# Kernel tuning notes

Hardware: AMD Instinct MI355X
Metric: run time of the kernel (lower is better)

## Reference

```python
import jax, jax.numpy as jnp
import numpy as np

B, T, D, H, E, K = 4, 1024, 1024, 16, 8, 2
HS = D // H
DFF = 4 * D
N = B * T
CAP_MAX = N * K // E  # static upper bound on expert capacity (all tokens non-skip)
SKIP_THR = 0.5
LN_EPS = 1e-5


def _ln(x, g, b):
    m = x.mean(-1, keepdims=True)
    v = x.var(-1, keepdims=True)  # biased, matches torch LayerNorm
    return (x - m) * jax.lax.rsqrt(v + LN_EPS) * g + b


def setup_inputs() -> dict:
    key = jax.random.key(0)
    ks = jax.random.split(key, 20)
    s = 0.02
    nrm = lambda k, shp: jax.random.normal(k, shp, dtype=jnp.float32) * s
    return {
        "x": jax.random.normal(ks[0], (B, T, D), dtype=jnp.float32),
        "noise": jax.random.normal(ks[1], (B, T, E), dtype=jnp.float32),
        "ln1_g": jnp.ones((D,), jnp.float32), "ln1_b": jnp.zeros((D,), jnp.float32),
        "wq": nrm(ks[2], (D, D)), "wk": nrm(ks[3], (D, D)), "wv": nrm(ks[4], (D, D)),
        "w_proj": nrm(ks[5], (D, D)), "b_proj": jnp.zeros((D,), jnp.float32),
        "ln2_g": jnp.ones((D,), jnp.float32), "ln2_b": jnp.zeros((D,), jnp.float32),
        "w_router": nrm(ks[6], (D, E)), "b_router": jnp.zeros((E,), jnp.float32),
        "w_noise": nrm(ks[7], (D, E)), "b_noise": jnp.zeros((E,), jnp.float32),
        "w_skip": nrm(ks[8], (D, 1)), "b_skip": jnp.zeros((1,), jnp.float32),
        "ew1": nrm(ks[9], (E, D, DFF)), "eb1": jnp.zeros((E, DFF), jnp.float32),
        "ew2": nrm(ks[10], (E, DFF, D)), "eb2": jnp.zeros((E, D), jnp.float32),
    }


def _block(x, noise, ln1_g, ln1_b, wq, wk, wv, w_proj, b_proj, ln2_g, ln2_b,
           w_router, b_router, w_noise, b_noise, w_skip, b_skip, ew1, eb1, ew2, eb2):
    # ---- multi-head causal self-attention (dropout is identity in eval) ----
    h = _ln(x, ln1_g, ln1_b)
    q = (h @ wq).reshape(B, T, H, HS)
    k = (h @ wk).reshape(B, T, H, HS)
    v = (h @ wv).reshape(B, T, H, HS)
    # NOTE: original scales by C**-0.5 with C = n_embed (not head_size)
    wei = jnp.einsum("bqhd,bkhd->bhqk", q, k) * (D ** -0.5)
    tril = jnp.tril(jnp.ones((T, T), bool))
    wei = jnp.where(tril, wei, -jnp.inf)
    wei = jax.nn.softmax(wei, axis=-1)
    attn = jnp.einsum("bhqk,bkhd->bqhd", wei, v).reshape(B, T, D)
    x1 = x + attn @ w_proj + b_proj

    # ---- cross-layer sparse MoE with skip routing ----
    h2 = _ln(x1, ln2_g, ln2_b)
    logits = h2 @ w_router + b_router                      # [B,T,E]
    noisy = logits + noise * jax.nn.softplus(h2 @ w_noise + b_noise)
    vals, idx = jax.lax.top_k(noisy, K)                    # [B,T,K]
    sparse = jnp.full_like(noisy, -jnp.inf)
    bi = jnp.arange(B)[:, None, None]
    ti = jnp.arange(T)[None, :, None]
    sparse = sparse.at[bi, ti, idx].set(vals)
    gates = jax.nn.softmax(sparse, axis=-1)                # [B,T,E]
    skip = (jax.nn.sigmoid(h2 @ w_skip + b_skip)[..., 0] > SKIP_THR)  # [B,T]

    fx = h2.reshape(N, D)
    fg = gates.reshape(N, E)
    fi = idx.reshape(N, K)
    nsk = ~skip.reshape(N)                                  # non-skip tokens
    n_ns = nsk.sum()
    capacity = (n_ns * K) // E                              # floor(tokens*K/E * 1.0)

    # per-expert dispatch with first-come capacity truncation (flat-token order)
    mask = (fi[None, :, :] == jnp.arange(E)[:, None, None]).any(-1) & nsk[None, :]  # [E,N]
    rank = jnp.cumsum(mask, axis=1) - 1                     # arrival order among non-skip
    within = mask & (rank < capacity)
    slot = jnp.where(within, rank, CAP_MAX)
    buf = jnp.full((E, CAP_MAX + 1), N, dtype=jnp.int32)
    buf = buf.at[jnp.arange(E)[:, None], slot].set(jnp.arange(N, dtype=jnp.int32)[None, :])
    tok = buf[:, :CAP_MAX]                                  # [E,CAP_MAX] token id or N (pad)
    valid = tok < N

    xp = jnp.concatenate([fx, jnp.zeros((1, D), fx.dtype)], axis=0)
    xin = xp[tok]                                           # [E,CAP_MAX,D]
    mid = jax.nn.relu(jnp.einsum("ecd,edf->ecf", xin, ew1) + eb1[:, None, :])
    yout = jnp.einsum("ecf,efd->ecd", mid, ew2) + eb2[:, None, :]
    gp = jnp.concatenate([fg, jnp.zeros((1, E), fg.dtype)], axis=0)
    gsel = gp[tok, jnp.arange(E)[:, None]]                  # [E,CAP_MAX]
    wout = yout * (gsel * valid)[..., None]

    updates = jnp.zeros((N + 1, D), fx.dtype).at[tok.reshape(-1)].add(wout.reshape(-1, D))[:N]
    moe_out = jnp.where(nsk[:, None], updates, fx).reshape(B, T, D)  # skipped tokens pass ln2(x1) through
    return x1 + moe_out


def reference(x, noise, ln1_g, ln1_b, wq, wk, wv, w_proj, b_proj, ln2_g, ln2_b,
              w_router, b_router, w_noise, b_noise, w_skip, b_skip, ew1, eb1, ew2, eb2):
    return _block(x, noise, ln1_g, ln1_b, wq, wk, wv, w_proj, b_proj, ln2_g, ln2_b,
                  w_router, b_router, w_noise, b_noise, w_skip, b_skip, ew1, eb1, ew2, eb2)
```

## Files before the change

kernel.cpp:

```cpp
#include <hip/hip_runtime.h>
#include <math.h>

#define TOK_N   4096
#define DMODEL  1024
#define NEXP    8
#define DFFD    4096
#define CAPMAX  1024

typedef __bf16 bf16x8 __attribute__((ext_vector_type(8)));
typedef __bf16 bf16x4 __attribute__((ext_vector_type(4)));
typedef float  f32x4  __attribute__((ext_vector_type(4)));

__device__ __forceinline__ f32x4 MFMA16(bf16x8 a, bf16x8 b, f32x4 c){
  return __builtin_amdgcn_mfma_f32_16x16x32_bf16(a, b, c, 0, 0, 0);
}

__device__ __forceinline__ void gl16(const __bf16* g, __bf16* l){
  __builtin_amdgcn_global_load_lds(
      (const __attribute__((address_space(1))) unsigned int*)g,
      (__attribute__((address_space(3))) unsigned int*)l, 16, 0, 0);
}

__device__ __forceinline__ float wave_sum(float x){
  #pragma unroll
  for (int o=32;o;o>>=1) x += __shfl_down(x,o);
  return x;
}

__global__ __launch_bounds__(256) void prep_kernel(
    const float* __restrict__ wq, const float* __restrict__ wk,
    const float* __restrict__ wv, const float* __restrict__ wp,
    __bf16* __restrict__ dh, __bf16* __restrict__ dl,
    const float* __restrict__ x, const float* __restrict__ g1,
    const float* __restrict__ b1, __bf16* __restrict__ hh, __bf16* __restrict__ hl)
{
  __shared__ float smem[64*65];
  int b = blockIdx.x, t = threadIdx.x;
  if (b < 1024){
    int z = b >> 8, rem = b & 255;
    int k0 = (rem >> 4) * 64, n0 = (rem & 15) * 64;
    const float* in = z==0?wq: z==1?wk: z==2?wv: wp;
    __bf16* oh = dh + (size_t)z*DMODEL*DMODEL;
    __bf16* ol = dl + (size_t)z*DMODEL*DMODEL;
    float (*tile)[65] = (float(*)[65])smem;
    #pragma unroll
    for (int i=0;i<4;i++){
      int row = (t>>4) + i*16, col = (t&15)*4;
      f32x4 f = __builtin_nontemporal_load((const f32x4*)&in[(size_t)(k0+row)*DMODEL + n0 + col]);
      tile[row][col]=f[0]; tile[row][col+1]=f[1]; tile[row][col+2]=f[2]; tile[row][col+3]=f[3];
    }
    __syncthreads();
    #pragma unroll
    for (int i=0;i<2;i++){
      int c = t + i*256;
      int orow = c>>3, kg = (c&7)*8;
      bf16x8 hv, lv;
      #pragma unroll
      for (int u=0;u<8;u++){
        float xv = tile[kg+u][orow];
        __bf16 hb = (__bf16)xv;
        hv[u]=hb; lv[u]=(__bf16)(xv-(float)hb);
      }
      *(bf16x8*)&oh[(size_t)(n0+orow)*DMODEL + k0 + kg] = hv;
      *(bf16x8*)&ol[(size_t)(n0+orow)*DMODEL + k0 + kg] = lv;
    }
  } else {
    int n = b - 1024;
    float4 v = ((const float4*)(x + (size_t)n*DMODEL))[t];
    float s  = v.x+v.y+v.z+v.w;
    float sq = v.x*v.x+v.y*v.y+v.z*v.z+v.w*v.w;
    s = wave_sum(s); sq = wave_sum(sq);
    int lane = t & 63, wid = t >> 6;
    if (lane==0){ smem[wid]=s; smem[8+wid]=sq; }
    __syncthreads();
    if (t==0){
      float a = smem[0]+smem[1]+smem[2]+smem[3];
      float c = smem[8]+smem[9]+smem[10]+smem[11];
      float mean = a*(1.0f/DMODEL);
      float var  = c*(1.0f/DMODEL) - mean*mean;
      smem[16] = mean; smem[17] = 1.0f/sqrtf(var + 1e-5f);
    }
    __syncthreads();
    float mean = smem[16], rstd = smem[17];
    float4 g4 = ((const float4*)g1)[t];
    float4 b4 = ((const float4*)b1)[t];
    float o_[4];
    o_[0] = (v.x-mean)*rstd*g4.x + b4.x;
    o_[1] = (v.y-mean)*rstd*g4.y + b4.y;
    o_[2] = (v.z-mean)*rstd*g4.z + b4.z;
    o_[3] = (v.w-mean)*rstd*g4.w + b4.w;
    bf16x4 h4, l4;
    #pragma unroll
    for (int i=0;i<4;i++){ __bf16 hb=(__bf16)o_[i]; h4[i]=hb; l4[i]=(__bf16)(o_[i]-(float)hb); }
    *(bf16x4*)&hh[(size_t)n*DMODEL + t*4] = h4;
    *(bf16x4*)&hl[(size_t)n*DMODEL + t*4] = l4;
  }
}

__global__ __launch_bounds__(256) void ln_router_kernel(
    const float* __restrict__ p0, const float* __restrict__ p1,
    const float* __restrict__ xres, const float* __restrict__ bproj,
    const float* __restrict__ g, const float* __restrict__ b,
    __bf16* __restrict__ oh, __bf16* __restrict__ ol, float* __restrict__ out,
    const float* __restrict__ wr, const float* __restrict__ br,
    const float* __restrict__ wn, const float* __restrict__ bn,
    const float* __restrict__ wsk, const float* __restrict__ bsk,
    const float* __restrict__ noise,
    int* __restrict__ idx2, float* __restrict__ gate2, int* __restrict__ nskv)
{
  int n = blockIdx.x, t = threadIdx.x;
  size_t ro = (size_t)n*DMODEL/4 + t;
  float4 a  = ((const float4*)p0)[ro];
  float4 a1 = ((const float4*)p1)[ro];
  float4 xr = ((const float4*)xres)[ro];
  float4 bp = ((const float4*)bproj)[t];
  float4 v;
  v.x = a.x+a1.x+xr.x+bp.x; v.y = a.y+a1.y+xr.y+bp.y;
  v.z = a.z+a1.z+xr.z+bp.z; v.w = a.w+a1.w+xr.w+bp.w;
  float s  = v.x+v.y+v.z+v.w;
  float sq = v.x*v.x+v.y*v.y+v.z*v.z+v.w*v.w;
  s = wave_sum(s); sq = wave_sum(sq);
  __shared__ float r1[4], r2[4];
  __shared__ float mean_s, rstd_s, sk_s;
  int lane = t & 63, wid = t >> 6;
  if (lane==0){ r1[wid]=s; r2[wid]=sq; }
  __syncthreads();
  if (t==0){
    float aa = r1[0]+r1[1]+r1[2]+r1[3];
    float cc = r2[0]+r2[1]+r2[2]+r2[3];
    float mean = aa*(1.0f/DMODEL);
    float var  = cc*(1.0f/DMODEL) - mean*mean;
    mean_s = mean; rstd_s = 1.0f/sqrtf(var + 1e-5f);
  }
  __syncthreads();
  float mean = mean_s, rstd = rstd_s;
  float4 g4 = ((const float4*)g)[t];
  float4 b4 = ((const float4*)b)[t];
  float o_[4];
  o_[0] = (v.x-mean)*rstd*g4.x + b4.x;
  o_[1] = (v.y-mean)*rstd*g4.y + b4.y;
  o_[2] = (v.z-mean)*rstd*g4.z + b4.z;
  o_[3] = (v.w-mean)*rstd*g4.w + b4.w;
  bf16x4 h4, l4;
  #pragma unroll
  for (int i=0;i<4;i++){ __bf16 hb=(__bf16)o_[i]; h4[i]=hb; l4[i]=(__bf16)(o_[i]-(float)hb); }
  *(bf16x4*)&oh[(size_t)n*DMODEL + t*4] = h4;
  *(bf16x4*)&ol[(size_t)n*DMODEL + t*4] = l4;
  int d0 = t*4;
  const float* wrp = wr + (size_t)d0*NEXP;
  const float* wnp = wn + (size_t)d0*NEXP;
  const float* wsp = wsk + d0;
  float vals[17];
  #pragma unroll
  for (int i=0;i<17;i++) vals[i]=0.f;
  #pragma unroll
  for (int i=0;i<4;i++){
    #pragma unroll
    for (int e=0;e<NEXP;e++){
      vals[e]   += o_[i]*wrp[i*NEXP+e];
      vals[8+e] += o_[i]*wnp[i*NEXP+e];
    }
    vals[16] += o_[i]*wsp[i];
  }
  __shared__ float red[4][17];
  #pragma unroll
  for (int i=0;i<17;i++){
    float xx = wave_sum(vals[i]);
    if (lane==0) red[wid][i] = xx;
  }
  __syncthreads();
  if (t==0){
    float noisy[NEXP];
    #pragma unroll
    for (int e=0;e<NEXP;e++){
      float lr = red[0][e]+red[1][e]+red[2][e]+red[3][e] + br[e];
      float pn = red[0][8+e]+red[1][8+e]+red[2][8+e]+red[3][8+e] + bn[e];
      float sp = fmaxf(pn,0.f) + log1pf(expf(-fabsf(pn)));
      noisy[e] = lr + noise[(size_t)n*NEXP + e]*sp;
    }
    float sk = red[0][16]+red[1][16]+red[2][16]+red[3][16] + bsk[0];
    sk_s = sk;
    nskv[n] = (sk <= 0.f) ? 1 : 0;
    int i0=0; float v0=noisy[0];
    #pragma unroll
    for (int e=1;e<NEXP;e++) if (noisy[e] > v0){ v0=noisy[e]; i0=e; }
    int i1=-1; float v1=-INFINITY;
    #pragma unroll
    for (int e=0;e<NEXP;e++) if (e!=i0 && noisy[e] > v1){ v1=noisy[e]; i1=e; }
    float tt = expf(v1 - v0);
    idx2[n*2+0]=i0; idx2[n*2+1]=i1;
    gate2[n*2+0]=1.0f/(1.0f+tt); gate2[n*2+1]=tt/(1.0f+tt);
  }
  __syncthreads();
  if (sk_s > 0.f){
    v.x += o_[0]; v.y += o_[1]; v.z += o_[2]; v.w += o_[3];
  }
  ((float4*)out)[ro] = v;
}

__global__ __launch_bounds__(256) void tconv_group(
    const float* __restrict__ ew1, const float* __restrict__ ew2,
    __bf16* __restrict__ e1T, __bf16* __restrict__ e2T, int e0, int G)
{
  __shared__ float tile[64][65];
  int z = blockIdx.z, t = threadIdx.x;
  const float* in; __bf16* out; int K, N, k0, n0;
  if (z < G){
    in = ew1 + (size_t)(e0+z)*DMODEL*DFFD; out = e1T + (size_t)z*DFFD*DMODEL;
    K = DMODEL; N = DFFD; k0 = blockIdx.y*64; n0 = blockIdx.x*64;
  } else {
    in = ew2 + (size_t)(e0+z-G)*DFFD*DMODEL; out = e2T + (size_t)(z-G)*DMODEL*DFFD;
    K = DFFD; N = DMODEL; k0 = blockIdx.x*64; n0 = blockIdx.y*64;
  }
  #pragma unroll
  for (int i=0;i<4;i++){
    int row = (t>>4) + i*16, col = (t&15)*4;
    f32x4 f = __builtin_nontemporal_load((const f32x4*)&in[(size_t)(k0+row)*N + n0 + col]);
    tile[row][col]=f[0]; tile[row][col+1]=f[1]; tile[row][col+2]=f[2]; tile[row][col+3]=f[3];
  }
  __syncthreads();
  #pragma unroll
  for (int i=0;i<2;i++){
    int c = t + i*256;
    int orow = c>>3, kg = (c&7)*8;
    bf16x8 hv;
    #pragma unroll
    for (int u=0;u<8;u++) hv[u] = (__bf16)tile[kg+u][orow];
    __builtin_nontemporal_store(hv, (bf16x8*)&out[(size_t)(n0+orow)*K + k0 + kg]);
  }
}

__global__ __launch_bounds__(256) void btrans_kernel(
    const __bf16* __restrict__ ih, const __bf16* __restrict__ il, int istride, int icol0,
    __bf16* __restrict__ oh, __bf16* __restrict__ ol){
  __shared__ __bf16 th[64][72], tl[64][72];
  int r0 = blockIdx.x*64, c0 = blockIdx.y*64;
  int t = threadIdx.x;
  {
    int r = t>>2, cg = (t&3)*16;
    size_t go = (size_t)(r0+r)*istride + icol0 + c0 + cg;
    *(bf16x8*)&th[r][cg]   = *(const bf16x8*)&ih[go];
    *(bf16x8*)&th[r][cg+8] = *(const bf16x8*)&ih[go+8];
    *(bf16x8*)&tl[r][cg]   = *(const bf16x8*)&il[go];
    *(bf16x8*)&tl[r][cg+8] = *(const bf16x8*)&il[go+8];
  }
  __syncthreads();
  {
    int c = t>>2, rg = (t&3)*16;
    bf16x8 a,b,e,f;
    #pragma unroll
    for (int u=0;u<8;u++){ a[u]=th[rg+u][c]; b[u]=th[rg+8+u][c]; e[u]=tl[rg+u][c]; f[u]=tl[rg+8+u][c]; }
    size_t go = (size_t)(c0+c)*TOK_N + r0 + rg;
    *(bf16x8*)&oh[go]   = a;
    *(bf16x8*)&oh[go+8] = b;
    *(bf16x8*)&ol[go]   = e;
    *(bf16x8*)&ol[go+8] = f;
  }
}

template<int MODE, bool SPLIT>
__global__ __launch_bounds__(256) void mgemm(
    const __bf16* __restrict__ Ah, const __bf16* __restrict__ Al, int Astride,
    const __bf16* __restrict__ Bh, const __bf16* __restrict__ Bl, int Bstride,
    const float* __restrict__ bias,
    float* __restrict__ Cf, __bf16* __restrict__ Ch, __bf16* __restrict__ Cl,
    int N, int K,
    const int* __restrict__ tok, const __bf16* __restrict__ zbuf)
{
  if constexpr (MODE==2){
    int z = blockIdx.z;
    Bh  += (size_t)z*((size_t)DFFD*DMODEL);
    bias+= (size_t)z*DFFD;
    Ch  += (size_t)z*((size_t)CAPMAX*DFFD);
    tok += z*CAPMAX;
  }
  if constexpr (MODE==4){
    int ge = blockIdx.z>>2, kz = blockIdx.z&3;
    Ah  += (size_t)ge*((size_t)CAPMAX*DFFD) + kz*1024;
    Bh  += (size_t)ge*((size_t)DMODEL*DFFD) + kz*1024;
    Cf  += (size_t)blockIdx.z*((size_t)CAPMAX*DMODEL);
    tok += ge*CAPMAX;
  }
  if constexpr (MODE==5){
    int kz = blockIdx.z;
    Ah += kz*512; Al += kz*512; Bh += kz*512; Bl += kz*512;
    Cf += (size_t)kz*((size_t)TOK_N*DMODEL);
  }
  int m0 = blockIdx.y*128, n0 = blockIdx.x*128;
  if ((MODE==2||MODE==4) && tok[m0] >= TOK_N) return;
  __shared__ __align__(16) __bf16 sAh[2*128*32], sBh[2*128*32];
  __shared__ __align__(16) __bf16 sAl[SPLIT?2*128*32:8], sBl[SPLIT?2*128*32:8];
  int t = threadIdx.x, lane = t&63, w = t>>6;
  int wr = w>>1, wc = w&1, fr = lane&15, kb = lane>>4;

  const __bf16* aB[2]; const __bf16* aBl[2]; bool aval[2];
  const __bf16* bB[2]; const __bf16* bBl[2];
  #pragma unroll
  for (int j=0;j<2;j++){
    int c = j*256 + w*64 + lane;
    int row = c>>2, grp = c&3;
    int sg = grp ^ ((row>>1)&3);
    if (MODE==2){
      int token = tok[m0+row];
      if (token < TOK_N){ aB[j] = Ah + (size_t)token*Astride + sg*8; aval[j]=true; }
      else              { aB[j] = zbuf + sg*8;                       aval[j]=false; }
    } else {
      aB[j] = Ah + (size_t)(m0+row)*Astride + sg*8; aval[j]=true;
      if (SPLIT) aBl[j] = Al + (size_t)(m0+row)*Astride + sg*8;
    }
    bB[j] = Bh + (size_t)(n0+row)*Bstride + sg*8;
    if (SPLIT) bBl[j] = Bl + (size_t)(n0+row)*Bstride + sg*8;
  }

  auto stage = [&](int buf, int kt){
    int base = buf*(128*32);
    #pragma unroll
    for (int j=0;j<2;j++){
      int cb8 = base + (j*256 + w*64)*8;
      gl16(aB[j] + (aval[j]? kt : 0), &sAh[cb8]);
      gl16(bB[j] + kt, &sBh[cb8]);
      if constexpr (SPLIT){
        gl16(aBl[j] + kt, &sAl[cb8]);
        gl16(bBl[j] + kt, &sBl[cb8]);
      }
    }
  };

  f32x4 acc[4][4];
  #pragma unroll
  for (int mt=0;mt<4;mt++)
    #pragma unroll
    for (int nt=0;nt<4;nt++) acc[mt][nt] = (f32x4){0.f,0.f,0.f,0.f};

  int nk = K >> 5;
  stage(0, 0);
  stage(1, 32);
  int xk = (kb ^ ((fr>>1)&3))*8;
  for (int ik=0; ik<nk; ik++){
    int cur = ik & 1;
    if (ik+1 < nk){
      if constexpr (SPLIT) asm volatile("s_waitcnt vmcnt(8)" ::: "memory");
      else                 asm volatile("s_waitcnt vmcnt(4)" ::: "memory");
    } else {
      asm volatile("s_waitcnt vmcnt(0)" ::: "memory");
    }
    __builtin_amdgcn_s_barrier();
    int fb = cur*(128*32);
    bf16x8 aFh[4], bFh[4];
    bf16x8 aFl[SPLIT?4:1], bFl[SPLIT?4:1];
    #pragma unroll
    for (int mt=0;mt<4;mt++) aFh[mt] = *(const bf16x8*)&sAh[fb + (wr*64+mt*16+fr)*32 + xk];
    #pragma unroll
    for (int nt=0;nt<4;nt++) bFh[nt] = *(const bf16x8*)&sBh[fb + (wc*64+nt*16+fr)*32 + xk];
    if constexpr (SPLIT){
      #pragma unroll
      for (int mt=0;mt<4;mt++) aFl[mt] = *(const bf16x8*)&sAl[fb + (wr*64+mt*16+fr)*32 + xk];
      #pragma unroll
      for (int nt=0;nt<4;nt++) bFl[nt] = *(const bf16x8*)&sBl[fb + (wc*64+nt*16+fr)*32 + xk];
    }
    asm volatile("s_waitcnt lgkmcnt(0)" ::: "memory");
    __builtin_amdgcn_sched_barrier(0);
    __builtin_amdgcn_s_barrier();
    if (ik+2 < nk) stage(cur, (ik+2)<<5);
    __builtin_amdgcn_s_setprio(1);
    #pragma unroll
    for (int mt=0;mt<4;mt++)
      #pragma unroll
      for (int nt=0;nt<4;nt++)
        acc[mt][nt] = MFMA16(aFh[mt], bFh[nt], acc[mt][nt]);
    if constexpr (SPLIT){
      #pragma unroll
      for (int mt=0;mt<4;mt++)
        #pragma unroll
        for (int nt=0;nt<4;nt++){
          acc[mt][nt] = MFMA16(aFh[mt], bFl[nt], acc[mt][nt]);
          acc[mt][nt] = MFMA16(aFl[mt], bFh[nt], acc[mt][nt]);
        }
    }
    __builtin_amdgcn_s_setprio(0);
  }

  #pragma unroll
  for (int mt=0; mt<4; mt++){
    int r0 = m0 + wr*64 + mt*16 + (lane>>4)*4;
    #pragma unroll
    for (int nt=0; nt<4; nt++){
      int col = n0 + wc*64 + nt*16 + fr;
      f32x4 v = acc[mt][nt];
      if constexpr (MODE==0){
        #pragma unroll
        for (int jj=0;jj<4;jj++){
          float val = v[jj];
          __bf16 hb = (__bf16)val;
          size_t idx = (size_t)(r0+jj)*N + col;
          Ch[idx] = hb; Cl[idx] = (__bf16)(val-(float)hb);
        }
      } else if constexpr (MODE==2){
        float bs = bias[col];
        #pragma unroll
        for (int jj=0;jj<4;jj++)
          Ch[(size_t)(r0+jj)*N + col] = (__bf16)fmaxf(v[jj]+bs, 0.f);
      } else {
        #pragma unroll
        for (int jj=0;jj<4;jj++)
          Cf[(size_t)(r0+jj)*N + col] = v[jj];
      }
    }
  }
}

__global__ __launch_bounds__(256) void gather_kernel(const float* __restrict__ yk,
    const int* __restrict__ tsrc, const float* __restrict__ gselb,
    const float* __restrict__ eb2, int e0, int G, float* __restrict__ out)
{
  int n = blockIdx.x, t = threadIdx.x;
  int s0 = tsrc[n*2], s1 = tsrc[n*2+1];
  float4 o; bool any = false;
  #pragma unroll
  for (int kk=0; kk<2; kk++){
    int src = kk ? s1 : s0;
    if (src < 0) continue;
    int e = src >> 10;
    int ge = e - e0;
    if (ge < 0 || ge >= G) continue;
    int r = src & (CAPMAX-1);
    if (!any){ o = ((const float4*)(out + (size_t)n*DMODEL))[t]; any = true; }
    float g = gselb[src];
    float4 acc = ((const float4*)(eb2 + (size_t)e*DMODEL))[t];
    #pragma unroll
    for (int z=0; z<4; z++){
      float4 p = ((const float4*)(yk + ((size_t)(ge*4+z)*CAPMAX + r)*DMODEL))[t];
      acc.x+=p.x; acc.y+=p.y; acc.z+=p.z; acc.w+=p.w;
    }
    o.x += g*acc.x; o.y += g*acc.y; o.z += g*acc.z; o.w += g*acc.w;
  }
  if (any) ((float4*)(out + (size_t)n*DMODEL))[t] = o;
}

__global__ __launch_bounds__(256) void attn_mfma_kernel(
    const __bf16* __restrict__ qkvh, const __bf16* __restrict__ qkvl,
    const __bf16* __restrict__ vth, const __bf16* __restrict__ vtl,
    __bf16* __restrict__ oh, __bf16* __restrict__ ol)
{
  __shared__ __align__(16) __bf16 Kh[2][64*64], Kl[2][64*64], Vh[2][64*64], Vl[2][64*64];
  __shared__ __align__(16) __bf16 Pt[2][4][16*64];
  int qtA = blockIdx.x, qtB = qtA + 8;
  int bh = blockIdx.y;
  int batch = bh>>4, head = bh&15;
  int t = threadIdx.x, lane = t&63, w = t>>6;
  int g = lane>>4, fr = lane&15;
  int col0 = head*64;
  size_t qbaseA = (size_t)(batch*1024 + qtA*64);
  size_t qbaseB = (size_t)(batch*1024 + qtB*64);
  const int QKS = 3*DMODEL;
  const float scale = 0.03125f;

  bf16x8 bQhA[2], bQlA[2], bQhB[2], bQlB[2];
  {
    int qrow = w*16 + fr;
    size_t rbA = (qbaseA+qrow)*QKS + col0 + g*8;
    size_t rbB = (qbaseB+qrow)*QKS + col0 + g*8;
    bQhA[0] = *(const bf16x8*)&qkvh[rbA];
    bQhA[1] = *(const bf16x8*)&qkvh[rbA+32];
    bQlA[0] = *(const bf16x8*)&qkvl[rbA];
    bQlA[1] = *(const bf16x8*)&qkvl[rbA+32];
    bQhB[0] = *(const bf16x8*)&qkvh[rbB];
    bQhB[1] = *(const bf16x8*)&qkvh[rbB+32];
    bQlB[0] = *(const bf16x8*)&qkvl[rbB];
    bQlB[1] = *(const bf16x8*)&qkvl[rbB+32];
  }

  auto stageKV = [&](int buf, int kt){
    size_t kbase = (size_t)(batch*1024 + kt*64);
    #pragma unroll
    for (int j=0;j<2;j++){
      int c = j*256 + t, row = c>>3, seg = c&7;
      int lb = (j*256 + w*64)*8;
      size_t gk = (kbase+row)*QKS + 1024 + col0 + ((seg^(row&7))*8);
      gl16(qkvh+gk, &Kh[buf][lb]);
      gl16(qkvl+gk, &Kl[buf][lb]);
      size_t gv = (size_t)(col0+row)*TOK_N + kbase + ((seg^(row&7))*8);
      gl16(vth+gv, &Vh[buf][lb]);
      gl16(vtl+gv, &Vl[buf][lb]);
    }
  };

  float mA = -INFINITY, lA = 0.f, mB = -INFINITY, lB = 0.f;
  f32x4 oA[4], oB[4];
  #pragma unroll
  for (int nt=0;nt<4;nt++){ oA[nt]=(f32x4){0.f,0.f,0.f,0.f}; oB[nt]=(f32x4){0.f,0.f,0.f,0.f}; }

  auto process = [&](int cur, bool diag, bf16x8* bQh, bf16x8* bQl,
                     float& m_, float& l_, f32x4* o_){
    int ntmax = diag ? (w+1) : 4;
    f32x4 s[4];
    #pragma unroll
    for (int nt=0;nt<4;nt++) s[nt]=(f32x4){0.f,0.f,0.f,0.f};
    __builtin_amdgcn_s_setprio(1);
    #pragma unroll
    for (int ks=0; ks<2; ks++){
      #pragma unroll
      for (int nt=0; nt<4; nt++){
        if (nt < ntmax){
          int kvr = nt*16 + fr;
          int sc_ = (ks*4 + g) ^ (kvr&7);
          bf16x8 aKh = *(const bf16x8*)&Kh[cur][kvr*64 + sc_*8];
          bf16x8 aKl = *(const bf16x8*)&Kl[cur][kvr*64 + sc_*8];
          s[nt] = MFMA16(aKh, bQh[ks], s[nt]);
          s[nt] = MFMA16(aKl, bQh[ks], s[nt]);
          s[nt] = MFMA16(aKh, bQl[ks], s[nt]);
        }
      }
    }
    __builtin_amdgcn_s_setprio(0);
    float sv[4][4];
    float mx = -INFINITY;
    int ql = w*16 + fr;
    #pragma unroll
    for (int nt=0;nt<4;nt++)
      #pragma unroll
      for (int j=0;j<4;j++){
        float xv = s[nt][j]*scale;
        if (nt >= ntmax || (diag && (nt*16 + g*4 + j) > ql)) xv = -INFINITY;
        sv[nt][j] = xv;
        mx = fmaxf(mx, xv);
      }
    mx = fmaxf(mx, __shfl_xor(mx,16));
    mx = fmaxf(mx, __shfl_xor(mx,32));
    float nm = fmaxf(m_, mx);
    float scf = __expf(m_ - nm);
    float ps = 0.f;
    #pragma unroll
    for (int nt=0;nt<4;nt++)
      #pragma unroll
      for (int j=0;j<4;j++){
        float p = __expf(sv[nt][j] - nm);
        sv[nt][j] = p;
        ps += p;
      }
    ps += __shfl_xor(ps,16);
    ps += __shfl_xor(ps,32);
    l_ = l_*scf + ps;
    m_ = nm;
    #pragma unroll
    for (int nt=0;nt<4;nt++) o_[nt] = o_[nt]*scf;
    #pragma unroll
    for (int nt=0;nt<4;nt++){
      bf16x4 hv, lv;
      #pragma unroll
      for (int j=0;j<4;j++){
        float pv = sv[nt][j];
        __bf16 hb = (__bf16)pv;
        hv[j] = hb; lv[j] = (__bf16)(pv-(float)hb);
      }
      int el = fr*64 + (((2*nt + (g>>1)) ^ (fr&7))*8) + (g&1)*4;
      *(bf16x4*)&Pt[0][w][el] = hv;
      *(bf16x4*)&Pt[1][w][el] = lv;
    }
    int ksmax = (diag && w < 2) ? 1 : 2;
    __builtin_amdgcn_s_setprio(1);
    #pragma unroll
    for (int ks=0; ks<2; ks++){
      if (ks < ksmax){
        int pc = (4*ks + g) ^ (fr&7);
        bf16x8 bPh = *(const bf16x8*)&Pt[0][w][fr*64 + pc*8];
        bf16x8 bPl = *(const bf16x8*)&Pt[1][w][fr*64 + pc*8];
        #pragma unroll
        for (int nt=0; nt<4; nt++){
          int vr = nt*16 + fr;
          int vc = (ks*4 + g) ^ (vr&7);
          bf16x8 aVh = *(const bf16x8*)&Vh[cur][vr*64 + vc*8];
          bf16x8 aVl = *(const bf16x8*)&Vl[cur][vr*64 + vc*8];
          o_[nt] = MFMA16(aVh, bPh, o_[nt]);
          o_[nt] = MFMA16(aVl, bPh, o_[nt]);
          o_[nt] = MFMA16(aVh, bPl, o_[nt]);
        }
      }
    }
    __builtin_amdgcn_s_setprio(0);
  };

  stageKV(0, 0);
  for (int kt=0; kt<=qtB; kt++){
    int cur = kt&1;
    __syncthreads();
    if (kt < qtB) stageKV(cur^1, kt+1);
    if (kt <= qtA) process(cur, kt==qtA, bQhA, bQlA, mA, lA, oA);
    process(cur, kt==qtB, bQhB, bQlB, mB, lB, oB);
  }

  auto writeOut = [&](size_t qbase, float l_, f32x4* o_){
    float inv = 1.0f/l_;
    #pragma unroll
    for (int nt=0;nt<4;nt++){
      bf16x4 hv, lv;
      #pragma unroll
      for (int j=0;j<4;j++){
        float val = o_[nt][j]*inv;
        __bf16 hb = (__bf16)val;
        hv[j] = hb; lv[j] = (__bf16)(val-(float)hb);
      }
      int el = fr*64 + (((2*nt + (g>>1)) ^ (fr&7))*8) + (g&1)*4;
      *(bf16x4*)&Pt[0][w][el] = hv;
      *(bf16x4*)&Pt[1][w][el] = lv;
    }
    #pragma unroll
    for (int r=0;r<2;r++){
      int c = r*4 + g;
      int el = fr*64 + ((c ^ (fr&7))*8);
      bf16x8 vh = *(const bf16x8*)&Pt[0][w][el];
      bf16x8 vl = *(const bf16x8*)&Pt[1][w][el];
      size_t go = (qbase + w*16 + fr)*DMODEL + col0 + c*8;
      *(bf16x8*)&oh[go] = vh;
      *(bf16x8*)&ol[go] = vl;
    }
  };
  writeOut(qbaseA, lA, oA);
  writeOut(qbaseB, lB, oB);
}

__global__ __launch_bounds__(256) void scan_kernel(const int* __restrict__ idx2,
    const float* __restrict__ gate2, const int* __restrict__ nskv,
    int* __restrict__ tok, float* __restrict__ gsel, float* __restrict__ zbuf,
    int* __restrict__ tsrc)
{
  int t = threadIdx.x;
  for (int i=t; i<NEXP*CAPMAX; i+=256){ tok[i]=TOK_N; gsel[i]=0.f; }
  for (int i=t; i<2*TOK_N; i+=256) tsrc[i] = -1;
  for (int i=t; i<1024; i+=256) zbuf[i]=0.f;
  __shared__ int cnts[256][NEXP];
  __shared__ int nns_part[256];
  __shared__ int cap_s;
  int loc[NEXP];
  #pragma unroll
  for (int e=0;e<NEXP;e++) loc[e]=0;
  int nn=0, base = t*16;
  for (int u=0;u<16;u++){
    int n = base+u;
    if (nskv[n]){ nn++; loc[idx2[n*2]]++; loc[idx2[n*2+1]]++; }
  }
  #pragma unroll
  for (int e=0;e<NEXP;e++) cnts[t][e]=loc[e];
  nns_part[t]=nn;
  __syncthreads();
  if (t < NEXP){ int run=0; for (int i=0;i<256;i++){ int c=cnts[i][t]; cnts[i][t]=run; run+=c; } }
  if (t == NEXP){ int sum=0; for (int i=0;i<256;i++) sum+=nns_part[i]; cap_s = sum/4; }
  __syncthreads();
  int capacity = cap_s;
  int run[NEXP];
  #pragma unroll
  for (int e=0;e<NEXP;e++) run[e]=cnts[t][e];
  for (int u=0;u<16;u++){
    int n = base+u;
    if (!nskv[n]) continue;
    #pragma unroll
    for (int kk=0;kk<2;kk++){
      int e = idx2[n*2+kk];
      int r = run[e]++;
      if (r < capacity){
        tok[e*CAPMAX+r]=n; gsel[e*CAPMAX+r]=gate2[n*2+kk];
        tsrc[n*2+kk] = e*CAPMAX + r;
      }
    }
  }
}

extern "C" void kernel_launch(void* const* d_in, const int* in_sizes, int n_in,
                              void* d_out, int out_size, void* d_ws, size_t ws_size,
                              hipStream_t stream) {
  const float* x      = (const float*)d_in[0];
  const float* noise  = (const float*)d_in[1];
  const float* ln1_g  = (const float*)d_in[2];
  const float* ln1_b  = (const float*)d_in[3];
  const float* wq     = (const float*)d_in[4];
  const float* wk     = (const float*)d_in[5];
  const float* wv     = (const float*)d_in[6];
  const float* w_proj = (const float*)d_in[7];
  const float* b_proj = (const float*)d_in[8];
  const float* ln2_g  = (const float*)d_in[9];
  const float* ln2_b  = (const float*)d_in[10];
  const float* w_rout = (const float*)d_in[11];
  const float* b_rout = (const float*)d_in[12];
  const float* w_noi  = (const float*)d_in[13];
  const float* b_noi  = (const float*)d_in[14];
  const float* w_skip = (const float*)d_in[15];
  const float* b_skip = (const float*)d_in[16];
  const float* ew1    = (const float*)d_in[17];
  const float* eb1    = (const float*)d_in[18];
  const float* ew2    = (const float*)d_in[19];
  const float* eb2    = (const float*)d_in[20];
  float* out = (float*)d_out;

  char* ws = (char*)d_ws;
  const size_t MB = 1024*1024;
  __bf16* h_hi   = (__bf16*)(ws + 0*MB);
  __bf16* h_lo   = (__bf16*)(ws + 8*MB);
  __bf16* qkv_hi = (__bf16*)(ws + 16*MB);
  __bf16* qkv_lo = (__bf16*)(ws + 40*MB);
  __bf16* wAllT_h= (__bf16*)(ws + 64*MB);
  __bf16* wAllT_l= (__bf16*)(ws + 72*MB);
  __bf16* vt_hi  = (__bf16*)(ws + 81*MB);
  __bf16* vt_lo  = (__bf16*)(ws + 89*MB);
  float*  pP     = (float*) (ws + 16*MB);
  __bf16* ao_hi = h_hi, *ao_lo = h_lo;

  int G; size_t off_mid, off_yk, off_e1, off_e2, off_meta;
  if (ws_size >= (size_t)338*MB){
    G = 8;  off_mid = 16;  off_yk = 80;  off_e1 = 208; off_e2 = 272; off_meta = 336;
  } else if (ws_size >= (size_t)178*MB){
    G = 4;  off_mid = 16;  off_yk = 48;  off_e1 = 112; off_e2 = 144; off_meta = 176;
  } else {
    G = 2;  off_e1 = 16;  off_e2 = 32;  off_mid = 48;  off_yk = 64;  off_meta = 96;
  }
  __bf16* e1T = (__bf16*)(ws + off_e1*MB);
  __bf16* e2T = (__bf16*)(ws + off_e2*MB);
  __bf16* mid = (__bf16*)(ws + off_mid*MB);
  float*  yk  = (float*) (ws + off_yk*MB);
  char* meta = ws + off_meta*MB;
  int*   idx2  = (int*)  (meta);
  float* gate2 = (float*)(meta + 32*1024);
  int*   nskv  = (int*)  (meta + 64*1024);
  int*   tokb  = (int*)  (meta + 80*1024);
  float* gselb = (float*)(meta + 112*1024);
  float* zbuf  = (float*)(meta + 144*1024);
  int*   tsrc  = (int*)  (meta + 160*1024);

  dim3 blk(256);
  prep_kernel<<<5120, blk, 0, stream>>>(wq, wk, wv, w_proj, wAllT_h, wAllT_l,
                                        x, ln1_g, ln1_b, h_hi, h_lo);
  mgemm<0,true><<<dim3(24,32), blk, 0, stream>>>(h_hi, h_lo, DMODEL, wAllT_h, wAllT_l, DMODEL,
      nullptr, nullptr, qkv_hi, qkv_lo, 3*DMODEL, DMODEL, nullptr, nullptr);
  btrans_kernel<<<dim3(64,16), blk, 0, stream>>>(qkv_hi, qkv_lo, 3*DMODEL, 2048, vt_hi, vt_lo);
  attn_mfma_kernel<<<dim3(8,64), blk, 0, stream>>>(qkv_hi, qkv_lo, vt_hi, vt_lo, ao_hi, ao_lo);
  mgemm<5,true><<<dim3(8,32,2), blk, 0, stream>>>(ao_hi, ao_lo, DMODEL,
      wAllT_h + (size_t)3*DMODEL*DMODEL, wAllT_l + (size_t)3*DMODEL*DMODEL, DMODEL,
      nullptr, pP, nullptr, nullptr, DMODEL, 512, nullptr, nullptr);
  ln_router_kernel<<<TOK_N, blk, 0, stream>>>(pP, pP + (size_t)TOK_N*DMODEL, x, b_proj,
      ln2_g, ln2_b, h_hi, h_lo, out,
      w_rout, b_rout, w_noi, b_noi, w_skip, b_skip, noise, idx2, gate2, nskv);
  scan_kernel<<<1, blk, 0, stream>>>(idx2, gate2, nskv, tokb, gselb, zbuf, tsrc);
  int ngrp = NEXP / G;
  for (int grp=0; grp<ngrp; grp++){
    int e0 = grp*G;
    tconv_group<<<dim3(64,16,2*G), blk, 0, stream>>>(ew1, ew2, e1T, e2T, e0, G);
    mgemm<2,false><<<dim3(32,8,G), blk, 0, stream>>>(h_hi, nullptr, DMODEL,
        e1T, nullptr, DMODEL, eb1 + (size_t)e0*DFFD,
        nullptr, mid, nullptr, DFFD, DMODEL, tokb + e0*CAPMAX, (const __bf16*)zbuf);
    mgemm<4,false><<<dim3(8,8,4*G), blk, 0, stream>>>(mid, nullptr, DFFD,
        e2T, nullptr, DFFD, nullptr,
        yk, nullptr, nullptr, DMODEL, 1024, tokb + e0*CAPMAX, nullptr);
    gather_kernel<<<TOK_N, blk, 0, stream>>>(yk, tsrc, gselb, eb2, e0, G, out);
  }
}
```

Before: 504.6 us.

## Enlarge split-precision GEMM M-tile to 256 and interleave attention QK for two query tiles

For the split hi/lo GEMMs (QKV projection and output projection), the M tile grows from 128 to 256 rows, so each wave computes 8x4 MFMA tiles and each staged B tile is reused across twice as many rows. The grids are halved to match, and the vmcnt wait is raised to cover the extra A loads. In the attention kernel, the process step is split into a QK phase and a softmax/PV phase, so both query tiles' QK MFMAs are issued before either softmax, giving more independent work to overlap. This raises register and LDS use per block and halves the number of GEMM blocks, which may reduce occupancy or leave CUs idle.

```diff
diff --git a/kernel.cpp b/kernel.cpp
--- a/kernel.cpp
+++ b/kernel.cpp
@@ -267,6 +267,9 @@
     int N, int K,
     const int* __restrict__ tok, const __bf16* __restrict__ zbuf)
 {
+  constexpr int BM = SPLIT ? 256 : 128;
+  constexpr int AJ = BM/64;
+  constexpr int MT = BM/32;
   if constexpr (MODE==2){
     int z = blockIdx.z;
     Bh  += (size_t)z*((size_t)DFFD*DMODEL);
@@ -286,17 +289,17 @@
     Ah += kz*512; Al += kz*512; Bh += kz*512; Bl += kz*512;
     Cf += (size_t)kz*((size_t)TOK_N*DMODEL);
   }
-  int m0 = blockIdx.y*128, n0 = blockIdx.x*128;
+  int m0 = blockIdx.y*BM, n0 = blockIdx.x*128;
   if ((MODE==2||MODE==4) && tok[m0] >= TOK_N) return;
-  __shared__ __align__(16) __bf16 sAh[2*128*32], sBh[2*128*32];
-  __shared__ __align__(16) __bf16 sAl[SPLIT?2*128*32:8], sBl[SPLIT?2*128*32:8];
+  __shared__ __align__(16) __bf16 sAh[2*BM*32], sBh[2*128*32];
+  __shared__ __align__(16) __bf16 sAl[SPLIT?2*BM*32:8], sBl[SPLIT?2*128*32:8];
   int t = threadIdx.x, lane = t&63, w = t>>6;
   int wr = w>>1, wc = w&1, fr = lane&15, kb = lane>>4;
 
-  const __bf16* aB[2]; const __bf16* aBl[2]; bool aval[2];
+  const __bf16* aB[AJ]; const __bf16* aBl[AJ]; bool aval[AJ];
   const __bf16* bB[2]; const __bf16* bBl[2];
   #pragma unroll
-  for (int j=0;j<2;j++){
+  for (int j=0;j<AJ;j++){
     int c = j*256 + w*64 + lane;
     int row = c>>2, grp = c&3;
     int sg = grp ^ ((row>>1)&3);
@@ -308,27 +311,36 @@
       aB[j] = Ah + (size_t)(m0+row)*Astride + sg*8; aval[j]=true;
       if (SPLIT) aBl[j] = Al + (size_t)(m0+row)*Astride + sg*8;
     }
+  }
+  #pragma unroll
+  for (int j=0;j<2;j++){
+    int c = j*256 + w*64 + lane;
+    int row = c>>2, grp = c&3;
+    int sg = grp ^ ((row>>1)&3);
     bB[j] = Bh + (size_t)(n0+row)*Bstride + sg*8;
     if (SPLIT) bBl[j] = Bl + (size_t)(n0+row)*Bstride + sg*8;
   }
 
   auto stage = [&](int buf, int kt){
-    int base = buf*(128*32);
+    int baseA = buf*(BM*32);
+    int baseB = buf*(128*32);
+    #pragma unroll
+    for (int j=0;j<AJ;j++){
+      int cb8 = baseA + (j*256 + w*64)*8;
+      gl16(aB[j] + (aval[j]? kt : 0), &sAh[cb8]);
+      if constexpr (SPLIT) gl16(aBl[j] + kt, &sAl[cb8]);
+    }
     #pragma unroll
     for (int j=0;j<2;j++){
-      int cb8 = base + (j*256 + w*64)*8;
-      gl16(aB[j] + (aval[j]? kt : 0), &sAh[cb8]);
+      int cb8 = baseB + (j*256 + w*64)*8;
       gl16(bB[j] + kt, &sBh[cb8]);
-      if constexpr (SPLIT){
-        gl16(aBl[j] + kt, &sAl[cb8]);
-        gl16(bBl[j] + kt, &sBl[cb8]);
-      }
+      if constexpr (SPLIT) gl16(bBl[j] + kt, &sBl[cb8]);
     }
   };
 
-  f32x4 acc[4][4];
-  #pragma unroll
-  for (int mt=0;mt<4;mt++)
+  f32x4 acc[MT][4];
+  #pragma unroll
+  for (int mt=0;mt<MT;mt++)
     #pragma unroll
     for (int nt=0;nt<4;nt++) acc[mt][nt] = (f32x4){0.f,0.f,0.f,0.f};
 
@@ -339,24 +351,25 @@
   for (int ik=0; ik<nk; ik++){
     int cur = ik & 1;
     if (ik+1 < nk){
-      if constexpr (SPLIT) asm volatile("s_waitcnt vmcnt(8)" ::: "memory");
+      if constexpr (SPLIT) asm volatile("s_waitcnt vmcnt(12)" ::: "memory");
       else                 asm volatile("s_waitcnt vmcnt(4)" ::: "memory");
     } else {
       asm volatile("s_waitcnt vmcnt(0)" ::: "memory");
     }
     __builtin_amdgcn_s_barrier();
-    int fb = cur*(128*32);
-    bf16x8 aFh[4], bFh[4];
-    bf16x8 aFl[SPLIT?4:1], bFl[SPLIT?4:1];
-    #pragma unroll
-    for (int mt=0;mt<4;mt++) aFh[mt] = *(const bf16x8*)&sAh[fb + (wr*64+mt*16+fr)*32 + xk];
-    #pragma unroll
-    for (int nt=0;nt<4;nt++) bFh[nt] = *(const bf16x8*)&sBh[fb + (wc*64+nt*16+fr)*32 + xk];
+    int fbA = cur*(BM*32);
+    int fbB = cur*(128*32);
+    bf16x8 aFh[MT], bFh[4];
+    bf16x8 aFl[SPLIT?MT:1], bFl[SPLIT?4:1];
+    #pragma unroll
+    for (int mt=0;mt<MT;mt++) aFh[mt] = *(const bf16x8*)&sAh[fbA + (wr*(BM/2)+mt*16+fr)*32 + xk];
+    #pragma unroll
+    for (int nt=0;nt<4;nt++) bFh[nt] = *(const bf16x8*)&sBh[fbB + (wc*64+nt*16+fr)*32 + xk];
     if constexpr (SPLIT){
       #pragma unroll
-      for (int mt=0;mt<4;mt++) aFl[mt] = *(const bf16x8*)&sAl[fb + (wr*64+mt*16+fr)*32 + xk];
-      #pragma unroll
-      for (int nt=0;nt<4;nt++) bFl[nt] = *(const bf16x8*)&sBl[fb + (wc*64+nt*16+fr)*32 + xk];
+      for (int mt=0;mt<MT;mt++) aFl[mt] = *(const bf16x8*)&sAl[fbA + (wr*(BM/2)+mt*16+fr)*32 + xk];
+      #pragma unroll
+      for (int nt=0;nt<4;nt++) bFl[nt] = *(const bf16x8*)&sBl[fbB + (wc*64+nt*16+fr)*32 + xk];
     }
     asm volatile("s_waitcnt lgkmcnt(0)" ::: "memory");
     __builtin_amdgcn_sched_barrier(0);
@@ -364,13 +377,13 @@
     if (ik+2 < nk) stage(cur, (ik+2)<<5);
     __builtin_amdgcn_s_setprio(1);
     #pragma unroll
-    for (int mt=0;mt<4;mt++)
+    for (int mt=0;mt<MT;mt++)
       #pragma unroll
       for (int nt=0;nt<4;nt++)
         acc[mt][nt] = MFMA16(aFh[mt], bFh[nt], acc[mt][nt]);
     if constexpr (SPLIT){
       #pragma unroll
-      for (int mt=0;mt<4;mt++)
+      for (int mt=0;mt<MT;mt++)
         #pragma unroll
         for (int nt=0;nt<4;nt++){
           acc[mt][nt] = MFMA16(aFh[mt], bFl[nt], acc[mt][nt]);
@@ -381,8 +394,8 @@
   }
 
   #pragma unroll
-  for (int mt=0; mt<4; mt++){
-    int r0 = m0 + wr*64 + mt*16 + (lane>>4)*4;
+  for (int mt=0; mt<MT; mt++){
+    int r0 = m0 + wr*(BM/2) + mt*16 + (lane>>4)*4;
     #pragma unroll
     for (int nt=0; nt<4; nt++){
       int col = n0 + wc*64 + nt*16 + fr;
@@ -490,10 +503,8 @@
   #pragma unroll
   for (int nt=0;nt<4;nt++){ oA[nt]=(f32x4){0.f,0.f,0.f,0.f}; oB[nt]=(f32x4){0.f,0.f,0.f,0.f}; }
 
-  auto process = [&](int cur, bool diag, bf16x8* bQh, bf16x8* bQl,
-                     float& m_, float& l_, f32x4* o_){
+  auto qk = [&](int cur, bool diag, bf16x8* bQh, bf16x8* bQl, f32x4* s){
     int ntmax = diag ? (w+1) : 4;
-    f32x4 s[4];
     #pragma unroll
     for (int nt=0;nt<4;nt++) s[nt]=(f32x4){0.f,0.f,0.f,0.f};
     __builtin_amdgcn_s_setprio(1);
@@ -513,6 +524,10 @@
       }
     }
     __builtin_amdgcn_s_setprio(0);
+  };
+
+  auto smpv = [&](int cur, bool diag, f32x4* s, float& m_, float& l_, f32x4* o_){
+    int ntmax = diag ? (w+1) : 4;
     float sv[4][4];
     float mx = -INFINITY;
     int ql = w*16 + fr;
@@ -585,8 +600,12 @@
     int cur = kt&1;
     __syncthreads();
     if (kt < qtB) stageKV(cur^1, kt+1);
-    if (kt <= qtA) process(cur, kt==qtA, bQhA, bQlA, mA, lA, oA);
-    process(cur, kt==qtB, bQhB, bQlB, mB, lB, oB);
+    bool doA = (kt <= qtA);
+    f32x4 sA[4], sB[4];
+    if (doA) qk(cur, kt==qtA, bQhA, bQlA, sA);
+    qk(cur, kt==qtB, bQhB, bQlB, sB);
+    if (doA) smpv(cur, kt==qtA, sA, mA, lA, oA);
+    smpv(cur, kt==qtB, sB, mB, lB, oB);
   }
 
   auto writeOut = [&](size_t qbase, float l_, f32x4* o_){
@@ -728,11 +747,11 @@
   dim3 blk(256);
   prep_kernel<<<5120, blk, 0, stream>>>(wq, wk, wv, w_proj, wAllT_h, wAllT_l,
                                         x, ln1_g, ln1_b, h_hi, h_lo);
-  mgemm<0,true><<<dim3(24,32), blk, 0, stream>>>(h_hi, h_lo, DMODEL, wAllT_h, wAllT_l, DMODEL,
+  mgemm<0,true><<<dim3(24,16), blk, 0, stream>>>(h_hi, h_lo, DMODEL, wAllT_h, wAllT_l, DMODEL,
       nullptr, nullptr, qkv_hi, qkv_lo, 3*DMODEL, DMODEL, nullptr, nullptr);
   btrans_kernel<<<dim3(64,16), blk, 0, stream>>>(qkv_hi, qkv_lo, 3*DMODEL, 2048, vt_hi, vt_lo);
   attn_mfma_kernel<<<dim3(8,64), blk, 0, stream>>>(qkv_hi, qkv_lo, vt_hi, vt_lo, ao_hi, ao_lo);
-  mgemm<5,true><<<dim3(8,32,2), blk, 0, stream>>>(ao_hi, ao_lo, DMODEL,
+  mgemm<5,true><<<dim3(8,16,2), blk, 0, stream>>>(ao_hi, ao_lo, DMODEL,
       wAllT_h + (size_t)3*DMODEL*DMODEL, wAllT_l + (size_t)3*DMODEL*DMODEL, DMODEL,
       nullptr, pP, nullptr, nullptr, DMODEL, 512, nullptr, nullptr);
   ln_router_kernel<<<TOK_N, blk, 0, stream>>>(pP, pP + (size_t)TOK_N*DMODEL, x, b_proj,
```

Result: slower. 530.7 us (+5.2%).
